# Kernel tuning notes

Hardware: AMD Instinct MI355X
Metric: run time of the kernel (lower is better)

## Reference

```python
import jax, jax.numpy as jnp
import numpy as np

N_NODES = 100000


def _gcn_layer(x, W, b, src, dst, n):
    # h = x @ W  (small feature dims)
    h = x @ W
    # add self-loops (GCNConv default: add_self_loops=True, weight 1)
    loop = jnp.arange(n, dtype=src.dtype)
    s = jnp.concatenate([src, loop])
    d = jnp.concatenate([dst, loop])
    # symmetric degree normalization: deg over incoming edges (incl. self-loops)
    deg = jax.ops.segment_sum(jnp.ones_like(d, dtype=h.dtype), d, num_segments=n)
    dinv = jnp.where(deg > 0, jax.lax.rsqrt(deg), 0.0)
    norm = dinv[s] * dinv[d]  # [E+N]
    msg = h[s] * norm[:, None]  # gather + scale
    out = jax.ops.segment_sum(msg, d, num_segments=n)  # scatter-add aggregation
    return out + b


def setup_inputs() -> dict:
    key = jax.random.key(0)
    k1, k2, k3, k4 = jax.random.split(key, 4)
    x = jax.random.normal(k1, (N_NODES, 512), dtype=jnp.float32)
    edge_index = jax.random.randint(k2, (2, 3200000), 0, N_NODES, dtype=jnp.int32)
    W1 = jax.random.normal(k3, (512, 16), dtype=jnp.float32) * (1.0 / np.sqrt(512))
    b1 = jnp.zeros((16,), dtype=jnp.float32)
    W2 = jax.random.normal(k4, (16, 40), dtype=jnp.float32) * (1.0 / np.sqrt(16))
    b2 = jnp.zeros((40,), dtype=jnp.float32)
    return {"x": x, "edge_index": edge_index, "W1": W1, "b1": b1, "W2": W2, "b2": b2}


def reference(x, edge_index, W1, b1, W2, b2):
    n = x.shape[0]
    src, dst = edge_index[0], edge_index[1]
    h = jax.nn.relu(_gcn_layer(x, W1, b1, src, dst, n))
    # F.dropout(training=False) is identity in eval mode
    h = _gcn_layer(h, W2, b2, src, dst, n)
    return jax.nn.log_softmax(h, axis=1)
```

## Files before the change

kernel.cpp:

```cpp
#include <hip/hip_runtime.h>
#include <hip/hip_fp16.h>


#define NFEAT_IN 512
#define NF1 16
#define NF2 40
#define BK_LG 8
#define TILE 8192

__global__ void k_bhist(const int* __restrict__ dst, int* __restrict__ gbsz, int E, int nbk) {
  __shared__ int h[512];
  for (int i = threadIdx.x; i < nbk; i += 256) h[i] = 0;
  __syncthreads();
  int stride = gridDim.x * 256;
  for (int e = blockIdx.x * 256 + threadIdx.x; e < E; e += stride)
    atomicAdd(&h[dst[e] >> BK_LG], 1);
  __syncthreads();
  for (int i = threadIdx.x; i < nbk; i += 256)
    if (h[i]) atomicAdd(&gbsz[i], h[i]);
}

__global__ void k_scanb(const int* __restrict__ gbsz, int* __restrict__ boff,
                        int* __restrict__ gcur, int* __restrict__ rp,
                        int nbk, int n, int E) {
  __shared__ int s[512];
  int t = threadIdx.x;
  s[t] = (t < nbk) ? gbsz[t] : 0;
  __syncthreads();
  for (int o = 1; o < 512; o <<= 1) {
    int v = (t >= o) ? s[t - o] : 0;
    __syncthreads();
    s[t] += v;
    __syncthreads();
  }
  if (t < nbk) {
    int ex = s[t] - gbsz[t];
    boff[t] = ex;
    gcur[t] = ex;
  }
  if (t == 0) { boff[nbk] = E; rp[n] = E; }
}

__global__ void k_part(const int* __restrict__ src, const int* __restrict__ dst,
                       int* __restrict__ gcur, unsigned int* __restrict__ ebuf,
                       int E, int nbk) {
  __shared__ int hist[512];
  __shared__ int hbase[512];
  int chunk = (E + gridDim.x - 1) / gridDim.x;
  int beg = blockIdx.x * chunk;
  int end = min(E, beg + chunk);
  for (int t0 = beg; t0 < end; t0 += TILE) {
    int t1 = min(end, t0 + TILE);
    for (int i = threadIdx.x; i < nbk; i += 256) hist[i] = 0;
    __syncthreads();
    for (int i = t0 + threadIdx.x; i < t1; i += 256)
      atomicAdd(&hist[dst[i] >> BK_LG], 1);
    __syncthreads();
    for (int i = threadIdx.x; i < nbk; i += 256) {
      int c = hist[i];
      hbase[i] = c ? atomicAdd(&gcur[i], c) : 0;
      hist[i] = 0;
    }
    __syncthreads();
    for (int i = t0 + threadIdx.x; i < t1; i += 256) {
      int d = dst[i];
      int b = d >> BK_LG;
      int r = atomicAdd(&hist[b], 1);
      ebuf[hbase[b] + r] = ((unsigned)(d & ((1 << BK_LG) - 1)) << 17) | (unsigned)src[i];
    }
    __syncthreads();
  }
}

__global__ __launch_bounds__(256) void k_sortb(
    const unsigned int* __restrict__ ebuf, const int* __restrict__ boff,
    int* __restrict__ esrc, int* __restrict__ rp, float* __restrict__ dinv,
    int n) {
  __shared__ int hist[256];
  __shared__ int scan[256];
  __shared__ int cur[256];
  int b = blockIdx.x;
  int e0 = boff[b], e1 = boff[b + 1];
  hist[threadIdx.x] = 0;
  __syncthreads();
  for (int e = e0 + threadIdx.x; e < e1; e += 256)
    atomicAdd(&hist[ebuf[e] >> 17], 1);
  __syncthreads();
  scan[threadIdx.x] = hist[threadIdx.x];
  __syncthreads();
  for (int o = 1; o < 256; o <<= 1) {
    int v = (threadIdx.x >= o) ? scan[threadIdx.x - o] : 0;
    __syncthreads();
    scan[threadIdx.x] += v;
    __syncthreads();
  }
  int excl = scan[threadIdx.x] - hist[threadIdx.x];
  cur[threadIdx.x] = e0 + excl;
  int vg = (b << BK_LG) + threadIdx.x;
  if (vg < n) {
    rp[vg] = e0 + excl;
    dinv[vg] = rsqrtf((float)(hist[threadIdx.x] + 1));
  }
  __syncthreads();
  for (int e = e0 + threadIdx.x; e < e1; e += 256) {
    unsigned p = ebuf[e];
    int pos = atomicAdd(&cur[p >> 17], 1);
    esrc[pos] = (int)(p & 0x1FFFF);
  }
}

__global__ void k_gemm1(const float* __restrict__ x, const float* __restrict__ W1,
                        const float* __restrict__ dinv, __half* __restrict__ h1s, int n) {
  __shared__ float Wt[NF1][NFEAT_IN + 4];
  for (int i = threadIdx.x; i < NFEAT_IN * NF1; i += 256) {
    int k = i >> 4, f = i & 15;
    Wt[f][k] = W1[i];
  }
  __syncthreads();
  int tid = blockIdx.x * 256 + threadIdx.x;
  int v = tid >> 4, f = tid & 15;
  const float4* xr = (const float4*)(x + (size_t)v * NFEAT_IN);
  const float4* wr = (const float4*)(&Wt[f][0]);
  float acc = 0.f;
#pragma unroll 8
  for (int k4 = 0; k4 < NFEAT_IN / 4; ++k4) {
    float4 a = xr[k4], w = wr[k4];
    acc = fmaf(a.x, w.x, acc);
    acc = fmaf(a.y, w.y, acc);
    acc = fmaf(a.z, w.z, acc);
    acc = fmaf(a.w, w.w, acc);
  }
  h1s[tid] = __float2half(acc * dinv[v]);
}

__global__ __launch_bounds__(256) void k_agg1(
    const int* __restrict__ rp, const int* __restrict__ esrc,
    const __half* __restrict__ h, const float* __restrict__ dinv,
    const float* __restrict__ b1, __half* __restrict__ as2) {
  int t = blockIdx.x * 256 + threadIdx.x;
  int v = t >> 4, f = t & 15;
  int beg = rp[v], end = rp[v + 1];
  float sum = __half2float(h[t]);
  int e = beg;
  for (; e + 8 <= end; e += 8) {
    int s0 = esrc[e],     s1 = esrc[e + 1], s2 = esrc[e + 2], s3 = esrc[e + 3];
    int s4 = esrc[e + 4], s5 = esrc[e + 5], s6 = esrc[e + 6], s7 = esrc[e + 7];
    float a0 = __half2float(h[(size_t)s0 * NF1 + f]);
    float a1 = __half2float(h[(size_t)s1 * NF1 + f]);
    float a2 = __half2float(h[(size_t)s2 * NF1 + f]);
    float a3 = __half2float(h[(size_t)s3 * NF1 + f]);
    float a4 = __half2float(h[(size_t)s4 * NF1 + f]);
    float a5 = __half2float(h[(size_t)s5 * NF1 + f]);
    float a6 = __half2float(h[(size_t)s6 * NF1 + f]);
    float a7 = __half2float(h[(size_t)s7 * NF1 + f]);
    sum += ((a0 + a1) + (a2 + a3)) + ((a4 + a5) + (a6 + a7));
  }
  for (; e < end; ++e) sum += __half2float(h[(size_t)esrc[e] * NF1 + f]);
  float dv = dinv[v];
  float a = fmaf(dv, sum, b1[f]);
  as2[t] = __float2half((a > 0.f ? a : 0.f) * dv);
}

__global__ __launch_bounds__(256) void k_agg2fin(
    const int* __restrict__ rp, const int* __restrict__ esrc,
    const __half* __restrict__ h, const float* __restrict__ dinv,
    const float* __restrict__ W2, const float* __restrict__ b2,
    float* __restrict__ out) {
  __shared__ float W2s[NF1 * NF2];
  __shared__ float b2s[NF2];
  __shared__ float sa[256];
  for (int i = threadIdx.x; i < NF1 * NF2; i += 256) W2s[i] = W2[i];
  if (threadIdx.x < NF2) b2s[threadIdx.x] = b2[threadIdx.x];
  int t = blockIdx.x * 256 + threadIdx.x;
  int v = t >> 4, f = t & 15;
  int beg = rp[v], end = rp[v + 1];
  float sum = __half2float(h[t]);
  int e = beg;
  for (; e + 8 <= end; e += 8) {
    int s0 = esrc[e],     s1 = esrc[e + 1], s2 = esrc[e + 2], s3 = esrc[e + 3];
    int s4 = esrc[e + 4], s5 = esrc[e + 5], s6 = esrc[e + 6], s7 = esrc[e + 7];
    float a0 = __half2float(h[(size_t)s0 * NF1 + f]);
    float a1 = __half2float(h[(size_t)s1 * NF1 + f]);
    float a2 = __half2float(h[(size_t)s2 * NF1 + f]);
    float a3 = __half2float(h[(size_t)s3 * NF1 + f]);
    float a4 = __half2float(h[(size_t)s4 * NF1 + f]);
    float a5 = __half2float(h[(size_t)s5 * NF1 + f]);
    float a6 = __half2float(h[(size_t)s6 * NF1 + f]);
    float a7 = __half2float(h[(size_t)s7 * NF1 + f]);
    sum += ((a0 + a1) + (a2 + a3)) + ((a4 + a5) + (a6 + a7));
  }
  for (; e < end; ++e) sum += __half2float(h[(size_t)esrc[e] * NF1 + f]);
  sa[threadIdx.x] = dinv[v] * sum;
  __syncthreads();
  const float* av = &sa[(threadIdx.x >> 4) << 4];
  float z0 = b2s[f], z1 = b2s[f + 16], z2 = (f < 8) ? b2s[f + 32] : -1e30f;
#pragma unroll
  for (int ff = 0; ff < NF1; ++ff) {
    float a = av[ff];
    z0 = fmaf(a, W2s[ff * NF2 + f], z0);
    z1 = fmaf(a, W2s[ff * NF2 + f + 16], z1);
    if (f < 8) z2 = fmaf(a, W2s[ff * NF2 + f + 32], z2);
  }
  float m = fmaxf(fmaxf(z0, z1), z2);
#pragma unroll
  for (int o = 8; o > 0; o >>= 1) m = fmaxf(m, __shfl_xor(m, o, 16));
  float s = __expf(z0 - m) + __expf(z1 - m) + ((f < 8) ? __expf(z2 - m) : 0.f);
#pragma unroll
  for (int o = 8; o > 0; o >>= 1) s += __shfl_xor(s, o, 16);
  float ls = m + __logf(s);
  float* orow = out + (size_t)v * NF2;
  orow[f] = z0 - ls;
  orow[f + 16] = z1 - ls;
  if (f < 8) orow[f + 32] = z2 - ls;
}

extern "C" void kernel_launch(void* const* d_in, const int* in_sizes, int n_in,
                              void* d_out, int out_size, void* d_ws, size_t ws_size,
                              hipStream_t stream) {
  const float* x  = (const float*)d_in[0];
  const int*   ei = (const int*)d_in[1];
  const float* W1 = (const float*)d_in[2];
  const float* b1 = (const float*)d_in[3];
  const float* W2 = (const float*)d_in[4];
  const float* b2 = (const float*)d_in[5];
  int n = in_sizes[0] / NFEAT_IN;
  int E = in_sizes[1] / 2;
  const int* src = ei;
  const int* dst = ei + E;
  float* out = (float*)d_out;
  int nbk = ((n - 1) >> BK_LG) + 1;

  char* ws = (char*)d_ws;
  size_t off = 0;
  auto alloc = [&](size_t bytes) { size_t o = off; off = (off + bytes + 63) & ~63ULL; return o; };
  int*   gbsz = (int*)(ws + alloc(512 * 4));
  int*   boff = (int*)(ws + alloc(513 * 4));
  int*   gcur = (int*)(ws + alloc(512 * 4));
  int*   rp   = (int*)(ws + alloc((size_t)(n + 1) * 4));
  float* dinv = (float*)(ws + alloc((size_t)n * 4));
  unsigned int* ebuf = (unsigned int*)(ws + alloc((size_t)E * 4));
  int*   esrc = (int*)(ws + alloc((size_t)E * 4));
  __half* h1s = (__half*)(ws + alloc((size_t)n * NF1 * 2));
  __half* as2 = (__half*)(ws + alloc((size_t)n * NF1 * 2));

  hipMemsetAsync(gbsz, 0, 512 * 4, stream);

  k_bhist<<<1024, 256, 0, stream>>>(dst, gbsz, E, nbk);
  k_scanb<<<1, 512, 0, stream>>>(gbsz, boff, gcur, rp, nbk, n, E);
  k_part <<<256, 256, 0, stream>>>(src, dst, gcur, ebuf, E, nbk);
  k_sortb<<<nbk, 256, 0, stream>>>(ebuf, boff, esrc, rp, dinv, n);
  k_gemm1<<<((size_t)n * NF1) / 256, 256, 0, stream>>>(x, W1, dinv, h1s, n);
  k_agg1 <<<((size_t)n * NF1) / 256, 256, 0, stream>>>(rp, esrc, h1s, dinv, b1, as2);
  k_agg2fin<<<((size_t)n * NF1) / 256, 256, 0, stream>>>(rp, esrc, as2, dinv, W2, b2, out);
}
```

Baseline: 581.2 us.

## Compute first-layer GEMM with fp16 MFMA and LDS-staged, coalesced x tiles

The first-layer projection becomes a wave-level 16x16x32 fp16 MFMA computation. Each wave handles 16 nodes and stages their x rows into LDS as fp16 with coalesced float4 loads, with W1 also held in LDS as fp16. Previously every thread read a full 512-float row on its own, which gave poor coalescing and scalar FMA throughput. The trade-off is lower input precision (fp16 conversion of x and W1), and the code assumes n is a multiple of 16.

After: 488.7 us. -15.9%, faster.

```diff
diff --git a/kernel.cpp b/kernel.cpp
--- a/kernel.cpp
+++ b/kernel.cpp
@@ -7,6 +7,12 @@
 #define NF2 40
 #define BK_LG 8
 #define TILE 8192
+#define XSTR 264
+#define WSTR 520
+
+typedef _Float16 f16x8 __attribute__((ext_vector_type(8)));
+typedef _Float16 f16x4 __attribute__((ext_vector_type(4)));
+typedef float f32x4 __attribute__((ext_vector_type(4)));
 
 __global__ void k_bhist(const int* __restrict__ dst, int* __restrict__ gbsz, int E, int nbk) {
   __shared__ int h[512];
@@ -109,28 +115,51 @@
   }
 }
 
-__global__ void k_gemm1(const float* __restrict__ x, const float* __restrict__ W1,
-                        const float* __restrict__ dinv, __half* __restrict__ h1s, int n) {
-  __shared__ float Wt[NF1][NFEAT_IN + 4];
+__global__ __launch_bounds__(256) void k_gemm1(
+    const float* __restrict__ x, const float* __restrict__ W1,
+    const float* __restrict__ dinv, __half* __restrict__ h1s, int ntiles) {
+  __shared__ _Float16 Wt[NF1 * WSTR];
+  __shared__ _Float16 xs[4][16 * XSTR];
   for (int i = threadIdx.x; i < NFEAT_IN * NF1; i += 256) {
     int k = i >> 4, f = i & 15;
-    Wt[f][k] = W1[i];
-  }
-  __syncthreads();
-  int tid = blockIdx.x * 256 + threadIdx.x;
-  int v = tid >> 4, f = tid & 15;
-  const float4* xr = (const float4*)(x + (size_t)v * NFEAT_IN);
-  const float4* wr = (const float4*)(&Wt[f][0]);
-  float acc = 0.f;
-#pragma unroll 8
-  for (int k4 = 0; k4 < NFEAT_IN / 4; ++k4) {
-    float4 a = xr[k4], w = wr[k4];
-    acc = fmaf(a.x, w.x, acc);
-    acc = fmaf(a.y, w.y, acc);
-    acc = fmaf(a.z, w.z, acc);
-    acc = fmaf(a.w, w.w, acc);
-  }
-  h1s[tid] = __float2half(acc * dinv[v]);
+    Wt[f * WSTR + k] = (_Float16)W1[i];
+  }
+  __syncthreads();
+
+  int w = threadIdx.x >> 6;
+  int l = threadIdx.x & 63;
+  int tile = blockIdx.x * 4 + w;
+  if (tile >= ntiles) return;
+  int v0 = tile << 4;
+
+  int fr = l & 15;
+  int kb = l >> 4;
+  _Float16* xsw = &xs[w][0];
+  const _Float16* xrow = &xsw[fr * XSTR + (kb << 3)];
+  const _Float16* wrow = &Wt[fr * WSTR + (kb << 3)];
+
+  f32x4 acc = {0.f, 0.f, 0.f, 0.f};
+#pragma unroll
+  for (int half = 0; half < 2; ++half) {
+#pragma unroll
+    for (int i = 0; i < 16; ++i) {
+      float4 a = *(const float4*)&x[(size_t)(v0 + i) * NFEAT_IN + half * 256 + l * 4];
+      f16x4 hv = {(_Float16)a.x, (_Float16)a.y, (_Float16)a.z, (_Float16)a.w};
+      *(f16x4*)&xsw[i * XSTR + l * 4] = hv;
+    }
+#pragma unroll
+    for (int kk = 0; kk < 8; ++kk) {
+      f16x8 av = *(const f16x8*)&xrow[kk * 32];
+      f16x8 bv = *(const f16x8*)&wrow[half * 256 + kk * 32];
+      acc = __builtin_amdgcn_mfma_f32_16x16x32_f16(av, bv, acc, 0, 0, 0);
+    }
+  }
+  int rbase = kb << 2;
+#pragma unroll
+  for (int q = 0; q < 4; ++q) {
+    int v = v0 + rbase + q;
+    h1s[(size_t)v * NF1 + fr] = __float2half(acc[q] * dinv[v]);
+  }
 }
 
 __global__ __launch_bounds__(256) void k_agg1(
@@ -229,6 +258,7 @@
   const int* dst = ei + E;
   float* out = (float*)d_out;
   int nbk = ((n - 1) >> BK_LG) + 1;
+  int ntiles = n >> 4;
 
   char* ws = (char*)d_ws;
   size_t off = 0;
@@ -249,7 +279,7 @@
   k_scanb<<<1, 512, 0, stream>>>(gbsz, boff, gcur, rp, nbk, n, E);
   k_part <<<256, 256, 0, stream>>>(src, dst, gcur, ebuf, E, nbk);
   k_sortb<<<nbk, 256, 0, stream>>>(ebuf, boff, esrc, rp, dinv, n);
-  k_gemm1<<<((size_t)n * NF1) / 256, 256, 0, stream>>>(x, W1, dinv, h1s, n);
+  k_gemm1<<<(ntiles + 3) / 4, 256, 0, stream>>>(x, W1, dinv, h1s, ntiles);
   k_agg1 <<<((size_t)n * NF1) / 256, 256, 0, stream>>>(rp, esrc, h1s, dinv, b1, as2);
   k_agg2fin<<<((size_t)n * NF1) / 256, 256, 0, stream>>>(rp, esrc, as2, dinv, W2, b2, out);
 }
```
